# Kernel tuning notes

Measured on AMD Instinct MI355X. Metric: run time of the kernel, lower is better.

The kernel has to match this reference:

```python
import jax, jax.numpy as jnp
import numpy as np

K = 20      # neighbors per node
D_T = 32    # timestep embedding dim

def _timestep_embedding(t, dim):
    half = dim // 2
    freqs = jnp.exp(-jnp.log(10000.0) * jnp.arange(half, dtype=jnp.float32) / (half - 1))
    args = t[:, None] * freqs[None, :]
    return jnp.concatenate([jnp.sin(args), jnp.cos(args)], axis=-1)

def _knn(pos, k):
    # pos: [N,3] -> (sources, targets): [N*k] edge index lists
    r2 = jnp.sum(pos * pos, axis=-1)
    d2 = r2[:, None] + r2[None, :] - 2.0 * (pos @ pos.T)   # [N,N] squared distances
    n = pos.shape[0]
    d2 = d2 + 1e10 * jnp.eye(n, dtype=pos.dtype)           # exclude self
    d2 = jax.lax.stop_gradient(d2)                         # indices only, no grad path
    _, idx = jax.lax.top_k(-d2, k)                         # [N,k]
    targets = jnp.repeat(jnp.arange(n), k)
    sources = idx.reshape(-1)
    return sources, targets

def _forward(z, t, conditioning, Wc1, bc1, Wc2, bc2, Wc3, bc3, We1, be1, We2, be2, Wn1, bn1, Wn2, bn2, alpha, beta):
    B, N, _ = z.shape
    pos, vel, massf = z[..., :3], z[..., 3:6], z[..., 6:]
    t = t * jnp.ones((B,), z.dtype)
    temb = _timestep_embedding(t, D_T)                     # [B,32]
    cond = jnp.concatenate([temb, conditioning], axis=1)   # [B,36]
    h = jax.nn.gelu(cond @ Wc1 + bc1)
    h = jax.nn.gelu(h @ Wc2 + bc2)
    cond = h @ Wc3 + bc3                                   # [B,36]
    fs = massf + cond[:, None, :]                          # scalar node feats [B,N,36]

    def single(pos_b, vel_b, fs_b):
        src, tgt = _knn(pos_b, K)
        rel = pos_b[src] - pos_b[tgt]                      # [E,3]
        r2 = jnp.sum(rel * rel, axis=-1, keepdims=True)
        vs, vt = vel_b[src], vel_b[tgt]
        # rotation-invariant edge features
        inv = jnp.concatenate([
            fs_b[src], fs_b[tgt], r2,
            jnp.sum(vs * vt, -1, keepdims=True),
            jnp.sum(vs * rel, -1, keepdims=True),
            jnp.sum(vt * rel, -1, keepdims=True),
        ], axis=-1)                                        # [E,76]
        e = jax.nn.gelu(inv @ We1 + be1) @ We2 + be2       # [E,4]
        logit, smsg, c_rel, c_vel = e[:, 0], e[:, 1], e[:, 2], e[:, 3]
        # segment softmax over incoming edges of each target node
        m = jax.ops.segment_max(logit, tgt, num_segments=N)
        a = jnp.exp(logit - m[tgt])
        denom = jax.ops.segment_sum(a, tgt, num_segments=N)
        w = a / denom[tgt]
        # equivariant vector messages, invariant scalar messages
        vmsg = w[:, None] * (c_rel[:, None] * rel + c_vel[:, None] * vs)
        vagg = jax.ops.segment_sum(vmsg, tgt, num_segments=N)              # [N,3]
        sagg = jax.ops.segment_sum(w * smsg, tgt, num_segments=N)[:, None]  # [N,1]
        hn = jax.nn.gelu(jnp.concatenate([fs_b, sagg], axis=-1) @ Wn1 + bn1)
        sout = hn @ Wn2 + bn2                              # [N,1] 0e output
        pos_out = pos_b + alpha * vagg                     # 1o
        feat_out = jnp.concatenate([beta * vagg, sout], axis=-1)  # 1o + 0e
        return jnp.concatenate([pos_out, feat_out], axis=-1)      # [N,7]

    h_all = jax.vmap(single)(pos, vel, fs)
    return z + h_all

def setup_inputs():
    key = jax.random.key(0)
    ks = jax.random.split(key, 10)
    B, N = 2, 8192
    d_cond = D_T + 4          # 36
    e_in = 2 * d_cond + 4     # 76
    e_hid, n_hid = 128, 64
    g = lambda i, shp: jax.random.normal(ks[i], shp, jnp.float32) * 0.05
    return {
        "z": jax.random.normal(ks[0], (B, N, 7), jnp.float32),
        "t": jax.random.uniform(ks[1], (B,), jnp.float32),
        "conditioning": jax.random.normal(ks[2], (B, 4), jnp.float32),
        "mask": jnp.ones((B, N), dtype=bool),
        "Wc1": g(3, (d_cond, 4 * d_cond)), "bc1": jnp.zeros((4 * d_cond,), jnp.float32),
        "Wc2": g(4, (4 * d_cond, 4 * d_cond)), "bc2": jnp.zeros((4 * d_cond,), jnp.float32),
        "Wc3": g(5, (4 * d_cond, d_cond)), "bc3": jnp.zeros((d_cond,), jnp.float32),
        "We1": g(6, (e_in, e_hid)), "be1": jnp.zeros((e_hid,), jnp.float32),
        "We2": g(7, (e_hid, 4)), "be2": jnp.zeros((4,), jnp.float32),
        "Wn1": g(8, (d_cond + 1, n_hid)), "bn1": jnp.zeros((n_hid,), jnp.float32),
        "Wn2": g(9, (n_hid, 1)), "bn2": jnp.zeros((1,), jnp.float32),
        "alpha": jnp.float32(0.1), "beta": jnp.float32(0.1),
    }

def reference(z, t, conditioning, mask, Wc1, bc1, Wc2, bc2, Wc3, bc3, We1, be1, We2, be2, Wn1, bn1, Wn2, bn2, alpha, beta):
    # mask is unused (module docstring: does not support masking)
    return _forward(z, t, conditioning, Wc1, bc1, Wc2, bc2, Wc3, bc3, We1, be1, We2, be2, Wn1, bn1, Wn2, bn2, alpha, beta)
```

## Files before the change

kernel.cpp:

```cpp
#include <hip/hip_runtime.h>
#include <math.h>

#define NB 8192
#define BATCH 2
#define KNN 20
#define BN (BATCH*NB)
#define NE (BN*KNN)
#define GT 16
#define NG 8
#define BIG 3.0e38f

__device__ __forceinline__ float gelu_f(float x){
    float x3 = x*x*x;
    float a = 0.7978845608028654f*(x + 0.044715f*x3);
    float e2 = __expf(2.0f*a);
    float th = 1.0f - __fdividef(2.0f, e2+1.0f);
    return 0.5f*x*(1.0f+th);
}

__global__ __launch_bounds__(256) void prepcond_kernel(const float* __restrict__ z,
        const float* __restrict__ t,
        const float* __restrict__ conditioning,
        const float* __restrict__ Wc1, const float* __restrict__ bc1,
        const float* __restrict__ Wc2, const float* __restrict__ bc2,
        const float* __restrict__ Wc3, const float* __restrict__ bc3,
        const float* __restrict__ We1, const float* __restrict__ be1,
        const float* __restrict__ We2,
        const float* __restrict__ Wn1, const float* __restrict__ bn1,
        float4* __restrict__ pos4, float4* __restrict__ vel4,
        float* __restrict__ consts, float* __restrict__ pack){
    int tid = threadIdx.x;
    int g = blockIdx.x*256 + tid;
    const float* zp = z + (size_t)g*7;
    float x = zp[0], y = zp[1], zz = zp[2];
    float r2 = x*x + y*y + zz*zz;
    pos4[g] = make_float4(x, y, zz, r2);
    vel4[g] = make_float4(zp[3], zp[4], zp[5], zp[6]);

    if (blockIdx.x >= BATCH) return;
    int b = blockIdx.x;
    __shared__ float ci[36];
    __shared__ float h1[144];
    __shared__ float h2[144];
    __shared__ float cnd[36];
    float tv = t[b];
    if (tid < 16){
        float f = expf(-9.210340371976184f * (float)tid / 15.0f);
        float a = tv*f;
        ci[tid]    = sinf(a);
        ci[16+tid] = cosf(a);
    }
    if (tid < 4) ci[32+tid] = conditioning[b*4+tid];
    __syncthreads();
    if (tid < 144){
        float acc = bc1[tid];
        #pragma unroll
        for (int c=0;c<36;c++) acc += ci[c]*Wc1[c*144+tid];
        h1[tid] = gelu_f(acc);
    }
    __syncthreads();
    if (tid < 144){
        float acc = bc2[tid];
        #pragma unroll 36
        for (int c=0;c<144;c++) acc += h1[c]*Wc2[c*144+tid];
        h2[tid] = gelu_f(acc);
    }
    __syncthreads();
    if (tid < 36){
        float acc = bc3[tid];
        #pragma unroll 36
        for (int c=0;c<144;c++) acc += h2[c]*Wc3[c*36+tid];
        cnd[tid] = acc;
    }
    __syncthreads();
    if (tid < 128){
        float accC = be1[tid], s1 = 0.f, s2 = 0.f;
        #pragma unroll
        for (int c=0;c<36;c++){
            float w1 = We1[c*128+tid];
            float w2 = We1[(36+c)*128+tid];
            accC += cnd[c]*(w1+w2);
            s1 += w1; s2 += w2;
        }
        consts[b*128+tid] = accC;
        pack[tid*12 + b] = accC;
        if (b==0){
            consts[256+tid] = s1; consts[384+tid] = s2;
            pack[tid*12+2] = s1;
            pack[tid*12+3] = s2;
            pack[tid*12+4] = We1[72*128+tid];
            pack[tid*12+5] = We1[73*128+tid];
            pack[tid*12+6] = We1[74*128+tid];
            pack[tid*12+7] = We1[75*128+tid];
            pack[tid*12+8]  = We2[tid*4+0];
            pack[tid*12+9]  = We2[tid*4+1];
            pack[tid*12+10] = We2[tid*4+2];
            pack[tid*12+11] = We2[tid*4+3];
        }
    }
    if (tid < 64){
        float accD = bn1[tid], t1 = 0.f;
        #pragma unroll
        for (int c=0;c<36;c++){
            float w = Wn1[c*64+tid];
            accD += cnd[c]*w;
            t1 += w;
        }
        consts[512 + b*64 + tid] = accD;
        if (b==0) consts[640+tid] = t1;
    }
}

__global__ __launch_bounds__(256, 4) void knn_kernel(const float4* __restrict__ pos4,
                                                     int* __restrict__ nbr){
    __shared__ float4 sPos[GT*64];
    __shared__ float2 sCand[16*64];
    int tid = threadIdx.x;
    int w = tid >> 6, lane = tid & 63;
    int n0g = blockIdx.x * 16;
    int b = n0g >> 13;
    int n0 = n0g & (NB-1);
    const float4* __restrict__ P = pos4 + b*NB;

    int nw = n0 + w*4;
    float nx[4], ny[4], nz[4], acc[4];
    #pragma unroll
    for (int k=0;k<4;k++){
        float4 p = P[nw+k];
        nx[k] = -2.0f*p.x; ny[k] = -2.0f*p.y; nz[k] = -2.0f*p.z;
        acc[k] = BIG;
    }
    int selfTile = n0 >> 6;
    int sl0 = (n0 & 63) + w*4;

    float4 pre0 = P[(w*4    )*64 + lane];
    float4 pre1 = P[(w*4 + 1)*64 + lane];
    float4 pre2 = P[(w*4 + 2)*64 + lane];
    float4 pre3 = P[(w*4 + 3)*64 + lane];
    for (int g=0; g<NG; ++g){
        __syncthreads();
        sPos[(w*4    )*64 + lane] = pre0;
        sPos[(w*4 + 1)*64 + lane] = pre1;
        sPos[(w*4 + 2)*64 + lane] = pre2;
        sPos[(w*4 + 3)*64 + lane] = pre3;
        if (g+1 < NG){
            pre0 = P[((g+1)*GT + w*4    )*64 + lane];
            pre1 = P[((g+1)*GT + w*4 + 1)*64 + lane];
            pre2 = P[((g+1)*GT + w*4 + 2)*64 + lane];
            pre3 = P[((g+1)*GT + w*4 + 3)*64 + lane];
        }
        __syncthreads();
        int tbase = g*GT;
        #pragma unroll
        for (int t=0;t<GT;t++){
            float4 q = sPos[t*64 + lane];
            if (tbase + t != selfTile){
                #pragma unroll
                for (int k=0;k<4;k++){
                    float d2 = fmaf(nx[k],q.x, fmaf(ny[k],q.y, fmaf(nz[k],q.z, q.w)));
                    acc[k] = fminf(acc[k], d2);
                }
            } else {
                #pragma unroll
                for (int k=0;k<4;k++){
                    float d2 = fmaf(nx[k],q.x, fmaf(ny[k],q.y, fmaf(nz[k],q.z, q.w)));
                    if (lane == sl0 + k) d2 = BIG;
                    acc[k] = fminf(acc[k], d2);
                }
            }
        }
    }

    float T[4];
    #pragma unroll
    for (int k=0;k<4;k++){
        float v = acc[k];
        #pragma unroll
        for (int K=2; K<=64; K<<=1){
            #pragma unroll
            for (int j=K>>1; j>0; j>>=1){
                float o = __shfl_xor(v, j);
                bool keepmin = (((lane & j) == 0) == ((lane & K) == 0));
                float mn = fminf(v,o), mx = fmaxf(v,o);
                v = keepmin ? mn : mx;
            }
        }
        T[k] = __shfl(v, 19);
    }

    int cnt[4];
    #pragma unroll
    for (int k=0;k<4;k++) cnt[k] = 0;
    unsigned long long lt = (1ull << lane) - 1ull;

    pre0 = P[(w*4    )*64 + lane];
    pre1 = P[(w*4 + 1)*64 + lane];
    pre2 = P[(w*4 + 2)*64 + lane];
    pre3 = P[(w*4 + 3)*64 + lane];
    for (int g=0; g<NG; ++g){
        __syncthreads();
        sPos[(w*4    )*64 + lane] = pre0;
        sPos[(w*4 + 1)*64 + lane] = pre1;
        sPos[(w*4 + 2)*64 + lane] = pre2;
        sPos[(w*4 + 3)*64 + lane] = pre3;
        if (g+1 < NG){
            pre0 = P[((g+1)*GT + w*4    )*64 + lane];
            pre1 = P[((g+1)*GT + w*4 + 1)*64 + lane];
            pre2 = P[((g+1)*GT + w*4 + 2)*64 + lane];
            pre3 = P[((g+1)*GT + w*4 + 3)*64 + lane];
        }
        __syncthreads();
        int tbase = g*GT;
        #pragma unroll 4
        for (int t=0;t<GT;t++){
            int tile = tbase + t;
            float4 q = sPos[t*64 + lane];
            int j = (tile<<6) + lane;
            bool selft = (tile == selfTile);
            #pragma unroll
            for (int k=0;k<4;k++){
                float d2 = fmaf(nx[k],q.x, fmaf(ny[k],q.y, fmaf(nz[k],q.z, q.w)));
                bool hit = (d2 <= T[k]);
                if (selft && (lane == sl0 + k)) hit = false;
                unsigned long long m = __ballot(hit);
                if (m){
                    if (hit){
                        int off = cnt[k] + (int)__popcll(m & lt);
                        if (off < 64)
                            sCand[(w*4+k)*64 + off] = make_float2(d2, __int_as_float(j));
                    }
                    cnt[k] += (int)__popcll(m);
                }
            }
        }
    }

    #pragma unroll
    for (int k=0;k<4;k++){
        int m = cnt[k]; if (m > 64) m = 64;
        float d; int idx;
        if (lane < m){
            float2 e = sCand[(w*4+k)*64 + lane];
            d = e.x; idx = __float_as_int(e.y);
        } else { d = BIG; idx = 0x7f000000 + lane; }
        #pragma unroll
        for (int K=2; K<=64; K<<=1){
            #pragma unroll
            for (int j=K>>1; j>0; j>>=1){
                float od = __shfl_xor(d, j);
                int   oi = __shfl_xor(idx, j);
                bool pless = (od < d) || (od == d && oi < idx);
                bool keepmin = (((lane & j) == 0) == ((lane & K) == 0));
                if (pless == keepmin){ d = od; idx = oi; }
            }
        }
        if (lane < KNN) nbr[(size_t)(n0g + w*4 + k)*KNN + lane] = idx;
    }
}

__global__ __launch_bounds__(320) void edgenode_kernel(const float4* __restrict__ pos4,
        const float4* __restrict__ vel4,
        const int* __restrict__ nbr,
        const float* __restrict__ pack,
        const float* __restrict__ consts,
        const float* __restrict__ Wn1,
        const float* __restrict__ Wn2,
        const float* __restrict__ be2,
        const float* __restrict__ bn2,
        const float* __restrict__ alpha_p,
        const float* __restrict__ beta_p,
        const float* __restrict__ z,
        float* __restrict__ out){
    __shared__ float4 sP[384];
    __shared__ float sLg[320], sSm[320], sUx[320], sUy[320], sUz[320];
    __shared__ float sD[64], sT1[64], sW36[64], sWo[64];
    __shared__ float sMf[16];
    __shared__ float4 sAgg[16];
    __shared__ float sPart[320];

    int tid = threadIdx.x;
    bool bb = (blockIdx.x >= 512);
    for (int k=tid; k<384; k+=320) sP[k] = ((const float4*)pack)[k];
    if (tid < 64){
        sD[tid]   = consts[512 + (bb?64:0) + tid];
        sT1[tid]  = consts[640+tid];
        sW36[tid] = Wn1[36*64+tid];
        sWo[tid]  = Wn2[tid];
    }

    int e = blockIdx.x*320 + tid;
    int i = e / KNN;
    int ln = tid / KNN;
    int r  = tid - ln*KNN;
    int bbase = bb ? NB : 0;
    int s = nbr[e];
    float4 ps = pos4[bbase + s], pt = pos4[i];
    float4 vs = vel4[bbase + s], vt = vel4[i];
    if (r == 0) sMf[ln] = vt.w;

    float rx = ps.x - pt.x, ry = ps.y - pt.y, rz = ps.z - pt.z;
    float r2  = rx*rx + ry*ry + rz*rz;
    float vv  = vs.x*vt.x + vs.y*vt.y + vs.z*vt.z;
    float vsr = vs.x*rx + vs.y*ry + vs.z*rz;
    float vtr = vt.x*rx + vt.y*ry + vt.z*rz;
    float mfs = vs.w, mft = vt.w;
    __syncthreads();

    float a0 = be2[0], a1 = be2[1], a2 = be2[2], a3 = be2[3];
    #pragma unroll 4
    for (int h=0; h<128; h++){
        float4 A  = sP[h*3];
        float4 Bv = sP[h*3+1];
        float4 C  = sP[h*3+2];
        float base = bb ? A.y : A.x;
        float x = base + mfs*A.z + mft*A.w + r2*Bv.x + vv*Bv.y + vsr*Bv.z + vtr*Bv.w;
        float gx = gelu_f(x);
        a0 += gx*C.x; a1 += gx*C.y; a2 += gx*C.z; a3 += gx*C.w;
    }
    sLg[tid] = a0;
    sSm[tid] = a1;
    sUx[tid] = a2*rx + a3*vs.x;
    sUy[tid] = a2*ry + a3*vs.y;
    sUz[tid] = a2*rz + a3*vs.z;
    __syncthreads();

    if (tid < 16){
        int base = tid*KNN;
        float m = -BIG;
        #pragma unroll
        for (int q=0;q<KNN;q++) m = fmaxf(m, sLg[base+q]);
        float den=0.f, wx=0.f, wy=0.f, wz=0.f, wsm=0.f;
        #pragma unroll
        for (int q=0;q<KNN;q++){
            float a = __expf(sLg[base+q]-m);
            den += a;
            wsm += a*sSm[base+q];
            wx  += a*sUx[base+q];
            wy  += a*sUy[base+q];
            wz  += a*sUz[base+q];
        }
        float inv = __fdividef(1.0f, den);
        sAgg[tid] = make_float4(wx*inv, wy*inv, wz*inv, wsm*inv);
    }
    __syncthreads();

    {
        float mf = sMf[ln];
        float sg = sAgg[ln].w;
        float part = 0.f;
        #pragma unroll
        for (int h=r; h<64; h+=KNN){
            float x = sD[h] + mf*sT1[h] + sg*sW36[h];
            part += gelu_f(x)*sWo[h];
        }
        sPart[tid] = part;
    }
    __syncthreads();

    if (tid < 16){
        float sout = bn2[0];
        #pragma unroll
        for (int q=0;q<KNN;q++) sout += sPart[tid*KNN+q];
        int node = blockIdx.x*16 + tid;
        float alpha = alpha_p[0], beta = beta_p[0];
        float4 ag = sAgg[tid];
        const float* zp = z + (size_t)node*7;
        float* op = out + (size_t)node*7;
        op[0] = zp[0]*2.0f + alpha*ag.x;
        op[1] = zp[1]*2.0f + alpha*ag.y;
        op[2] = zp[2]*2.0f + alpha*ag.z;
        op[3] = zp[3] + beta*ag.x;
        op[4] = zp[4] + beta*ag.y;
        op[5] = zp[5] + beta*ag.z;
        op[6] = zp[6] + sout;
    }
}

extern "C" void kernel_launch(void* const* d_in, const int* in_sizes, int n_in,
                              void* d_out, int out_size, void* d_ws, size_t ws_size,
                              hipStream_t stream) {
    const float* z    = (const float*)d_in[0];
    const float* t    = (const float*)d_in[1];
    const float* cond = (const float*)d_in[2];
    const float* Wc1  = (const float*)d_in[4];
    const float* bc1  = (const float*)d_in[5];
    const float* Wc2  = (const float*)d_in[6];
    const float* bc2  = (const float*)d_in[7];
    const float* Wc3  = (const float*)d_in[8];
    const float* bc3  = (const float*)d_in[9];
    const float* We1  = (const float*)d_in[10];
    const float* be1  = (const float*)d_in[11];
    const float* We2  = (const float*)d_in[12];
    const float* be2  = (const float*)d_in[13];
    const float* Wn1  = (const float*)d_in[14];
    const float* bn1  = (const float*)d_in[15];
    const float* Wn2  = (const float*)d_in[16];
    const float* bn2  = (const float*)d_in[17];
    const float* alp  = (const float*)d_in[18];
    const float* bet  = (const float*)d_in[19];
    float* out = (float*)d_out;

    char* ws = (char*)d_ws;
    float4* pos4   = (float4*)(ws);
    float4* vel4   = (float4*)(ws + 262144);
    float*  consts = (float*)(ws + 524288);
    float*  pack   = (float*)(ws + 528384);
    int*    nbr    = (int*)(ws + 534528);

    prepcond_kernel<<<dim3(BN/256), dim3(256), 0, stream>>>(z, t, cond,
        Wc1, bc1, Wc2, bc2, Wc3, bc3, We1, be1, We2, Wn1, bn1,
        pos4, vel4, consts, pack);
    knn_kernel<<<dim3(BN/16), dim3(256), 0, stream>>>(pos4, nbr);
    edgenode_kernel<<<dim3(BN/16), dim3(320), 0, stream>>>(pos4, vel4, nbr, pack, consts,
        Wn1, Wn2, be2, bn2, alp, bet, z, out);
}
```

Before: 207.5 us.

## Widen kNN blocks to 512 threads and use packed float2 distance math

```diff
diff --git a/kernel.cpp b/kernel.cpp
--- a/kernel.cpp
+++ b/kernel.cpp
@@ -6,16 +6,17 @@
 #define KNN 20
 #define BN (BATCH*NB)
 #define NE (BN*KNN)
-#define GT 16
-#define NG 8
+#define GT 32
+#define NG 4
 #define BIG 3.0e38f
 
+typedef float f32x2 __attribute__((ext_vector_type(2)));
+
 __device__ __forceinline__ float gelu_f(float x){
-    float x3 = x*x*x;
-    float a = 0.7978845608028654f*(x + 0.044715f*x3);
-    float e2 = __expf(2.0f*a);
-    float th = 1.0f - __fdividef(2.0f, e2+1.0f);
-    return 0.5f*x*(1.0f+th);
+    float t = x*x;
+    float m = x*fmaf(t, -0.0713548163f, -1.5957691216f);
+    float e = __expf(m);
+    return __fdividef(x, 1.0f + e);
 }
 
 __global__ __launch_bounds__(256) void prepcond_kernel(const float* __restrict__ z,
@@ -111,25 +112,31 @@
     }
 }
 
-__global__ __launch_bounds__(256, 4) void knn_kernel(const float4* __restrict__ pos4,
+#define DIST4(q) \
+    f32x2 d01 = nx01*(q).x + (ny01*(q).y + (nz01*(q).z + (q).w)); \
+    f32x2 d23 = nx23*(q).x + (ny23*(q).y + (nz23*(q).z + (q).w));
+
+__global__ __launch_bounds__(512, 4) void knn_kernel(const float4* __restrict__ pos4,
                                                      int* __restrict__ nbr){
     __shared__ float4 sPos[GT*64];
-    __shared__ float2 sCand[16*64];
+    __shared__ float2 sCand[32*64];
     int tid = threadIdx.x;
     int w = tid >> 6, lane = tid & 63;
-    int n0g = blockIdx.x * 16;
+    int n0g = blockIdx.x * 32;
     int b = n0g >> 13;
     int n0 = n0g & (NB-1);
     const float4* __restrict__ P = pos4 + b*NB;
 
     int nw = n0 + w*4;
-    float nx[4], ny[4], nz[4], acc[4];
-    #pragma unroll
-    for (int k=0;k<4;k++){
-        float4 p = P[nw+k];
-        nx[k] = -2.0f*p.x; ny[k] = -2.0f*p.y; nz[k] = -2.0f*p.z;
-        acc[k] = BIG;
-    }
+    float4 p0 = P[nw], p1 = P[nw+1], p2 = P[nw+2], p3 = P[nw+3];
+    f32x2 nx01 = { -2.0f*p0.x, -2.0f*p1.x };
+    f32x2 ny01 = { -2.0f*p0.y, -2.0f*p1.y };
+    f32x2 nz01 = { -2.0f*p0.z, -2.0f*p1.z };
+    f32x2 nx23 = { -2.0f*p2.x, -2.0f*p3.x };
+    f32x2 ny23 = { -2.0f*p2.y, -2.0f*p3.y };
+    f32x2 nz23 = { -2.0f*p2.z, -2.0f*p3.z };
+    f32x2 acc01 = { BIG, BIG }, acc23 = { BIG, BIG };
+
     int selfTile = n0 >> 6;
     int sl0 = (n0 & 63) + w*4;
 
@@ -154,27 +161,23 @@
         #pragma unroll
         for (int t=0;t<GT;t++){
             float4 q = sPos[t*64 + lane];
-            if (tbase + t != selfTile){
-                #pragma unroll
-                for (int k=0;k<4;k++){
-                    float d2 = fmaf(nx[k],q.x, fmaf(ny[k],q.y, fmaf(nz[k],q.z, q.w)));
-                    acc[k] = fminf(acc[k], d2);
-                }
-            } else {
-                #pragma unroll
-                for (int k=0;k<4;k++){
-                    float d2 = fmaf(nx[k],q.x, fmaf(ny[k],q.y, fmaf(nz[k],q.z, q.w)));
-                    if (lane == sl0 + k) d2 = BIG;
-                    acc[k] = fminf(acc[k], d2);
-                }
+            DIST4(q)
+            if (tbase + t == selfTile){
+                if (lane == sl0    ) d01.x = BIG;
+                if (lane == sl0 + 1) d01.y = BIG;
+                if (lane == sl0 + 2) d23.x = BIG;
+                if (lane == sl0 + 3) d23.y = BIG;
             }
-        }
-    }
-
+            acc01.x = fminf(acc01.x, d01.x); acc01.y = fminf(acc01.y, d01.y);
+            acc23.x = fminf(acc23.x, d23.x); acc23.y = fminf(acc23.y, d23.y);
+        }
+    }
+
+    float accs[4] = { acc01.x, acc01.y, acc23.x, acc23.y };
     float T[4];
     #pragma unroll
     for (int k=0;k<4;k++){
-        float v = acc[k];
+        float v = accs[k];
         #pragma unroll
         for (int K=2; K<=64; K<<=1){
             #pragma unroll
@@ -185,7 +188,8 @@
                 v = keepmin ? mn : mx;
             }
         }
-        T[k] = __shfl(v, 19);
+        float t20 = __shfl(v, 19);
+        T[k] = t20 + fmaxf(fabsf(t20), 1.0f) * 4.0e-6f;
     }
 
     int cnt[4];
@@ -217,9 +221,11 @@
             float4 q = sPos[t*64 + lane];
             int j = (tile<<6) + lane;
             bool selft = (tile == selfTile);
+            DIST4(q)
+            float d2a[4] = { d01.x, d01.y, d23.x, d23.y };
             #pragma unroll
             for (int k=0;k<4;k++){
-                float d2 = fmaf(nx[k],q.x, fmaf(ny[k],q.y, fmaf(nz[k],q.z, q.w)));
+                float d2 = d2a[k];
                 bool hit = (d2 <= T[k]);
                 if (selft && (lane == sl0 + k)) hit = false;
                 unsigned long long m = __ballot(hit);
@@ -410,7 +416,7 @@
     prepcond_kernel<<<dim3(BN/256), dim3(256), 0, stream>>>(z, t, cond,
         Wc1, bc1, Wc2, bc2, Wc3, bc3, We1, be1, We2, Wn1, bn1,
         pos4, vel4, consts, pack);
-    knn_kernel<<<dim3(BN/16), dim3(256), 0, stream>>>(pos4, nbr);
+    knn_kernel<<<dim3(BN/32), dim3(512), 0, stream>>>(pos4, nbr);
     edgenode_kernel<<<dim3(BN/16), dim3(320), 0, stream>>>(pos4, vel4, nbr, pack, consts,
         Wn1, Wn2, be2, bn2, alp, bet, z, out);
 }
```

New measurement: 202.8 us. 2.3% less time.
